# Optimization experiments

Measured on AMD Instinct MI355X. Metric: run time of the kernel, lower is better.

Reference implementation:

```python
import jax, jax.numpy as jnp
import numpy as np

B, T, C, H = 128, 512, 128, 64  # batch, seq, n_embd, head_size


def setup_inputs() -> dict:
    key = jax.random.key(0)
    ks = jax.random.split(key, 6)
    s = 1.0 / np.sqrt(C)
    return {
        "x": jax.random.normal(ks[0], (B, T, C), dtype=jnp.float32),
        "Wg": jax.random.normal(ks[1], (C, C), dtype=jnp.float32) * s,
        "bg": jnp.zeros((C,), dtype=jnp.float32),
        "Wk": jax.random.normal(ks[2], (C, H), dtype=jnp.float32) * s,
        "Wq": jax.random.normal(ks[3], (C, H), dtype=jnp.float32) * s,
        "Wv": jax.random.normal(ks[4], (C, H), dtype=jnp.float32) * s,
    }


def reference(x, Wg, bg, Wk, Wq, Wv):
    # GateLayer: x * sigmoid(Linear(x))
    g = jax.nn.sigmoid(jnp.einsum('btc,cd->btd', x, Wg) + bg)
    xg = x * g
    k = jnp.einsum('btc,ch->bth', xg, Wk)
    q = jnp.einsum('btc,ch->bth', xg, Wq)
    v = jnp.einsum('btc,ch->bth', xg, Wv)
    # NOTE: original scales by C**-0.5 (n_embd), not head_size**-0.5
    scale = C ** -0.5
    wei = jnp.einsum('bqh,bkh->bqk', q, k) * scale  # [B,T,T]
    causal = jnp.tril(jnp.ones((T, T), dtype=bool))
    wei = jnp.where(causal, wei, -jnp.inf)
    wei = jax.nn.softmax(wei, axis=-1)
    # dropout is identity in eval mode
    out = jnp.einsum('bqk,bkh->bqh', wei, v)  # [B,T,H]
    return out
```

## Files before the change

kernel.cpp:

```cpp
#include <hip/hip_runtime.h>


#define BB 128
#define TB 512
#define CC 128
#define HH 64

static constexpr float SCALE = 0.088388347648318447f;

typedef __attribute__((ext_vector_type(8))) short bf16x8;
typedef __attribute__((ext_vector_type(8))) unsigned short u16x8;
typedef __attribute__((ext_vector_type(4))) float f32x4;

__device__ inline unsigned short f2bf(float f) {
    union { float f; unsigned u; } x; x.f = f;
    unsigned r = x.u + 0x7fff + ((x.u >> 16) & 1);
    return (unsigned short)(r >> 16);
}
__device__ inline float bf2f(unsigned short h) {
    union { unsigned u; float f; } x; x.u = ((unsigned)h) << 16;
    return x.f;
}

__global__ void prep_weights(const float* __restrict__ Wg, const float* __restrict__ Wk,
                             const float* __restrict__ Wq, const float* __restrict__ Wv,
                             unsigned short* __restrict__ WgT, unsigned short* __restrict__ WkT,
                             unsigned short* __restrict__ WqT, unsigned short* __restrict__ WvT)
{
    int idx = blockIdx.x * 256 + threadIdx.x;
    if (idx < 16384) {
        int n = idx >> 7, k = idx & 127;
        WgT[idx] = f2bf(Wg[k * CC + n]);
    } else {
        int j = idx - 16384;
        int mtx = j >> 13;
        int r = j & 8191;
        int n = r >> 7, k = r & 127;
        const float* W = (mtx == 0) ? Wk : (mtx == 1) ? Wq : Wv;
        unsigned short* WT = (mtx == 0) ? WkT : (mtx == 1) ? WqT : WvT;
        WT[r] = f2bf(W[k * HH + n]);
    }
}

__global__ __launch_bounds__(256, 3) void gate_qkv_kernel(
    const float* __restrict__ x, const float* __restrict__ bg,
    const unsigned short* __restrict__ WgT, const unsigned short* __restrict__ WkT,
    const unsigned short* __restrict__ WqT, const unsigned short* __restrict__ WvT,
    unsigned short* __restrict__ qo, unsigned short* __restrict__ ko,
    unsigned short* __restrict__ vto)
{
    __shared__ unsigned short xsb[128 * 136];

    const int tid  = threadIdx.x;
    const int wv   = tid >> 6;
    const int lane = tid & 63;
    const int l15  = lane & 15;
    const int quad = lane >> 4;
    const int R0   = blockIdx.x * 128;

#pragma unroll
    for (int it = 0; it < 16; ++it) {
        int fid = tid + 256 * it;
        int r = fid >> 5, c4 = fid & 31;
        float4 xv = *(const float4*)(x + (size_t)(R0 + r) * CC + c4 * 4);
        ushort4 h;
        h.x = f2bf(xv.x); h.y = f2bf(xv.y); h.z = f2bf(xv.z); h.w = f2bf(xv.w);
        *(ushort4*)(xsb + r * 136 + c4 * 4) = h;
    }
    __syncthreads();

    bf16x8 bx[2][4];
#pragma unroll
    for (int mt = 0; mt < 2; ++mt)
#pragma unroll
        for (int kc = 0; kc < 4; ++kc)
            bx[mt][kc] = *(const bf16x8*)(xsb + (32 * wv + 16 * mt + l15) * 136 +
                                          kc * 32 + quad * 8);

    f32x4 acc[8][2];
#pragma unroll
    for (int nt = 0; nt < 8; ++nt)
#pragma unroll
        for (int mt = 0; mt < 2; ++mt) acc[nt][mt] = (f32x4){0.f, 0.f, 0.f, 0.f};

#pragma unroll
    for (int nt = 0; nt < 8; ++nt) {
        bf16x8 aw[4];
#pragma unroll
        for (int kc = 0; kc < 4; ++kc)
            aw[kc] = *(const bf16x8*)(WgT + (16 * nt + l15) * CC + kc * 32 + quad * 8);
#pragma unroll
        for (int mt = 0; mt < 2; ++mt)
#pragma unroll
            for (int kc = 0; kc < 4; ++kc)
                acc[nt][mt] = __builtin_amdgcn_mfma_f32_16x16x32_bf16(
                    aw[kc], bx[mt][kc], acc[nt][mt], 0, 0, 0);
    }

#pragma unroll
    for (int nt = 0; nt < 8; ++nt) {
        float4 bgv = *(const float4*)(bg + 16 * nt + quad * 4);
#pragma unroll
        for (int mt = 0; mt < 2; ++mt) {
            int m = 32 * wv + 16 * mt + l15;
            unsigned short* p = xsb + m * 136 + 16 * nt + quad * 4;
            ushort4 xb = *(const ushort4*)p;
            float s0 = acc[nt][mt][0] + bgv.x;
            float s1 = acc[nt][mt][1] + bgv.y;
            float s2 = acc[nt][mt][2] + bgv.z;
            float s3 = acc[nt][mt][3] + bgv.w;
            ushort4 o;
            o.x = f2bf(bf2f(xb.x) / (1.f + __expf(-s0)));
            o.y = f2bf(bf2f(xb.y) / (1.f + __expf(-s1)));
            o.z = f2bf(bf2f(xb.z) / (1.f + __expf(-s2)));
            o.w = f2bf(bf2f(xb.w) / (1.f + __expf(-s3)));
            *(ushort4*)p = o;
        }
    }
    __syncthreads();

#pragma unroll
    for (int mt = 0; mt < 2; ++mt)
#pragma unroll
        for (int kc = 0; kc < 4; ++kc)
            bx[mt][kc] = *(const bf16x8*)(xsb + (32 * wv + 16 * mt + l15) * 136 +
                                          kc * 32 + quad * 8);

    const int b = R0 >> 9, t0 = R0 & 511;
    for (int pj = 0; pj < 3; ++pj) {
        const unsigned short* WT = (pj == 0) ? WkT : (pj == 1) ? WqT : WvT;
        f32x4 pacc[4][2];
#pragma unroll
        for (int nt = 0; nt < 4; ++nt)
#pragma unroll
            for (int mt = 0; mt < 2; ++mt) pacc[nt][mt] = (f32x4){0.f, 0.f, 0.f, 0.f};

#pragma unroll
        for (int nt = 0; nt < 4; ++nt) {
            bf16x8 aw[4];
#pragma unroll
            for (int kc = 0; kc < 4; ++kc)
                aw[kc] = *(const bf16x8*)(WT + (16 * nt + l15) * CC + kc * 32 + quad * 8);
#pragma unroll
            for (int mt = 0; mt < 2; ++mt)
#pragma unroll
                for (int kc = 0; kc < 4; ++kc)
                    pacc[nt][mt] = __builtin_amdgcn_mfma_f32_16x16x32_bf16(
                        aw[kc], bx[mt][kc], pacc[nt][mt], 0, 0, 0);
        }

        if (pj < 2) {
            unsigned short* O = (pj == 0) ? ko : qo;
#pragma unroll
            for (int nt = 0; nt < 4; ++nt)
#pragma unroll
                for (int mt = 0; mt < 2; ++mt) {
                    int m = 32 * wv + 16 * mt + l15;
                    ushort4 h;
                    h.x = f2bf(pacc[nt][mt][0]);
                    h.y = f2bf(pacc[nt][mt][1]);
                    h.z = f2bf(pacc[nt][mt][2]);
                    h.w = f2bf(pacc[nt][mt][3]);
                    *(ushort4*)(O + (size_t)(R0 + m) * HH + 16 * nt + quad * 4) = h;
                }
        } else {
#pragma unroll
            for (int nt = 0; nt < 4; ++nt)
#pragma unroll
                for (int mt = 0; mt < 2; ++mt) {
                    int m = 32 * wv + 16 * mt + l15;
                    unsigned short* dst =
                        vto + (size_t)b * (HH * TB) + (16 * nt + quad * 4) * TB + t0 + m;
#pragma unroll
                    for (int r = 0; r < 4; ++r)
                        dst[r * TB] = f2bf(pacc[nt][mt][r]);
                }
        }
    }
}

__global__ __launch_bounds__(256) void attn_kernel(
    const unsigned short* __restrict__ q, const unsigned short* __restrict__ k,
    const unsigned short* __restrict__ vt, float* __restrict__ out)
{
    __shared__ unsigned short ks[64 * 72];
    __shared__ unsigned short vs[64 * 72];
    __shared__ unsigned short ps[64 * 76];

    const int tid  = threadIdx.x;
    const int wave = tid >> 6;
    const int lane = tid & 63;
    const int l15  = lane & 15;
    const int quad = lane >> 4;
    const int pr   = blockIdx.x;
    const int b    = blockIdx.y;
    const size_t base = (size_t)b * TB * HH;

    for (int pass = 0; pass < 2; ++pass) {
        const int qt = pass ? (7 - pr) : pr;
        const int q0 = qt * 64;

        const unsigned short* qrow = q + base + (size_t)(q0 + 16 * wave + l15) * HH;
        bf16x8 aq0 = *(const bf16x8*)(qrow + quad * 8);
        bf16x8 aq1 = *(const bf16x8*)(qrow + 32 + quad * 8);

        f32x4 o4[4];
        float mrow[4], lrow[4];
#pragma unroll
        for (int nt = 0; nt < 4; ++nt) o4[nt] = (f32x4){0.f, 0.f, 0.f, 0.f};
#pragma unroll
        for (int r = 0; r < 4; ++r) { mrow[r] = -1e30f; lrow[r] = 0.f; }

        for (int kt = 0; kt <= qt; ++kt) {
            const int k0 = kt * 64;
            __syncthreads();
#pragma unroll
            for (int i = 0; i < 2; ++i) {
                int cid = tid + 256 * i;
                int r = cid >> 3, c8 = cid & 7;
                *(bf16x8*)(ks + r * 72 + c8 * 8) =
                    *(const bf16x8*)(k + base + (size_t)(k0 + r) * HH + c8 * 8);
                *(bf16x8*)(vs + r * 72 + c8 * 8) =
                    *(const bf16x8*)(vt + base + (size_t)r * TB + k0 + c8 * 8);
            }
            __syncthreads();

            f32x4 s[4];
#pragma unroll
            for (int nt = 0; nt < 4; ++nt) {
                bf16x8 bk0 = *(const bf16x8*)(ks + (16 * nt + l15) * 72 + quad * 8);
                bf16x8 bk1 = *(const bf16x8*)(ks + (16 * nt + l15) * 72 + 32 + quad * 8);
                f32x4 z = (f32x4){0.f, 0.f, 0.f, 0.f};
                z = __builtin_amdgcn_mfma_f32_16x16x32_bf16(aq0, bk0, z, 0, 0, 0);
                z = __builtin_amdgcn_mfma_f32_16x16x32_bf16(aq1, bk1, z, 0, 0, 0);
                s[nt] = z;
            }

            const bool diag = (kt == qt);
            float mx[4];
#pragma unroll
            for (int r = 0; r < 4; ++r) mx[r] = -1e30f;
#pragma unroll
            for (int nt = 0; nt < 4; ++nt)
#pragma unroll
                for (int r = 0; r < 4; ++r) {
                    float sv = s[nt][r] * SCALE;
                    if (diag && (16 * nt + l15) > (16 * wave + quad * 4 + r)) sv = -1e30f;
                    s[nt][r] = sv;
                    mx[r] = fmaxf(mx[r], sv);
                }

#pragma unroll
            for (int r = 0; r < 4; ++r) {
                mx[r] = fmaxf(mx[r], __shfl_xor(mx[r], 1));
                mx[r] = fmaxf(mx[r], __shfl_xor(mx[r], 2));
                mx[r] = fmaxf(mx[r], __shfl_xor(mx[r], 4));
                mx[r] = fmaxf(mx[r], __shfl_xor(mx[r], 8));
            }
            float alpha[4], psum[4];
#pragma unroll
            for (int r = 0; r < 4; ++r) {
                float mn = fmaxf(mrow[r], mx[r]);
                alpha[r] = __expf(mrow[r] - mn);
                mrow[r] = mn;
                psum[r] = 0.f;
            }
#pragma unroll
            for (int nt = 0; nt < 4; ++nt)
#pragma unroll
                for (int r = 0; r < 4; ++r) {
                    float e = __expf(s[nt][r] - mrow[r]);
                    psum[r] += e;
                    ps[(16 * wave + quad * 4 + r) * 76 + 16 * nt + l15] = f2bf(e);
                }
#pragma unroll
            for (int r = 0; r < 4; ++r) {
                psum[r] += __shfl_xor(psum[r], 1);
                psum[r] += __shfl_xor(psum[r], 2);
                psum[r] += __shfl_xor(psum[r], 4);
                psum[r] += __shfl_xor(psum[r], 8);
                lrow[r] = lrow[r] * alpha[r] + psum[r];
            }
#pragma unroll
            for (int nt = 0; nt < 4; ++nt)
#pragma unroll
                for (int r = 0; r < 4; ++r) o4[nt][r] *= alpha[r];

            bf16x8 ap0 = *(const bf16x8*)(ps + (16 * wave + l15) * 76 + quad * 8);
            bf16x8 ap1 = *(const bf16x8*)(ps + (16 * wave + l15) * 76 + 32 + quad * 8);
#pragma unroll
            for (int nt = 0; nt < 4; ++nt) {
                bf16x8 bv0 = *(const bf16x8*)(vs + (16 * nt + l15) * 72 + quad * 8);
                bf16x8 bv1 = *(const bf16x8*)(vs + (16 * nt + l15) * 72 + 32 + quad * 8);
                o4[nt] = __builtin_amdgcn_mfma_f32_16x16x32_bf16(ap0, bv0, o4[nt], 0, 0, 0);
                o4[nt] = __builtin_amdgcn_mfma_f32_16x16x32_bf16(ap1, bv1, o4[nt], 0, 0, 0);
            }
        }

        float inv[4];
#pragma unroll
        for (int r = 0; r < 4; ++r) inv[r] = 1.f / lrow[r];
#pragma unroll
        for (int nt = 0; nt < 4; ++nt)
#pragma unroll
            for (int r = 0; r < 4; ++r)
                out[base + (size_t)(q0 + 16 * wave + quad * 4 + r) * HH + 16 * nt + l15] =
                    o4[nt][r] * inv[r];
    }
}

extern "C" void kernel_launch(void* const* d_in, const int* in_sizes, int n_in,
                              void* d_out, int out_size, void* d_ws, size_t ws_size,
                              hipStream_t stream) {
    const float* x  = (const float*)d_in[0];
    const float* Wg = (const float*)d_in[1];
    const float* bg = (const float*)d_in[2];
    const float* Wk = (const float*)d_in[3];
    const float* Wq = (const float*)d_in[4];
    const float* Wv = (const float*)d_in[5];
    float* out = (float*)d_out;

    unsigned short* ws = (unsigned short*)d_ws;
    const size_t BTH = (size_t)BB * TB * HH;
    unsigned short* qo  = ws;
    unsigned short* ko  = ws + BTH;
    unsigned short* vto = ws + 2 * BTH;
    unsigned short* WgT = ws + 3 * BTH;
    unsigned short* WkT = WgT + 16384;
    unsigned short* WqT = WkT + 8192;
    unsigned short* WvT = WqT + 8192;

    hipLaunchKernelGGL(prep_weights, dim3(160), dim3(256), 0, stream,
                       Wg, Wk, Wq, Wv, WgT, WkT, WqT, WvT);
    hipLaunchKernelGGL(gate_qkv_kernel, dim3(BB * TB / 128), dim3(256), 0, stream,
                       x, bg, WgT, WkT, WqT, WvT, qo, ko, vto);
    hipLaunchKernelGGL(attn_kernel, dim3(4, BB), dim3(256), 0, stream,
                       qo, ko, vto, out);
}
```

Measured before the change: 137.5 us.

## Halve gate tile, stage V transpose through LDS, one query tile per attention block

The gate/QKV kernel now handles 64 rows per block instead of 128, with one 16-row MFMA tile per wave. This drops the second __syncthreads and lets occupancy rise to 4 blocks. V is written transposed through shared memory so the global stores become 16-byte vectors instead of scattered 2-byte stores, and the sigmoid divide is replaced by a hardware reciprocal. The attention kernel drops the paired-tile load-balancing scheme and launches 8 query tiles per batch, one per block. This doubles the grid size but makes block work uneven, ordered heaviest first.

```diff
diff --git a/kernel.cpp b/kernel.cpp
--- a/kernel.cpp
+++ b/kernel.cpp
@@ -42,24 +42,24 @@
     }
 }
 
-__global__ __launch_bounds__(256, 3) void gate_qkv_kernel(
+__global__ __launch_bounds__(256, 4) void gate_qkv_kernel(
     const float* __restrict__ x, const float* __restrict__ bg,
     const unsigned short* __restrict__ WgT, const unsigned short* __restrict__ WkT,
     const unsigned short* __restrict__ WqT, const unsigned short* __restrict__ WvT,
     unsigned short* __restrict__ qo, unsigned short* __restrict__ ko,
     unsigned short* __restrict__ vto)
 {
-    __shared__ unsigned short xsb[128 * 136];
+    __shared__ unsigned short xsb[64 * 136];
 
     const int tid  = threadIdx.x;
     const int wv   = tid >> 6;
     const int lane = tid & 63;
     const int l15  = lane & 15;
     const int quad = lane >> 4;
-    const int R0   = blockIdx.x * 128;
-
-#pragma unroll
-    for (int it = 0; it < 16; ++it) {
+    const int R0   = blockIdx.x * 64;
+
+#pragma unroll
+    for (int it = 0; it < 8; ++it) {
         int fid = tid + 256 * it;
         int r = fid >> 5, c4 = fid & 31;
         float4 xv = *(const float4*)(x + (size_t)(R0 + r) * CC + c4 * 4);
@@ -69,117 +69,93 @@
     }
     __syncthreads();
 
-    bf16x8 bx[2][4];
-#pragma unroll
-    for (int mt = 0; mt < 2; ++mt)
-#pragma unroll
-        for (int kc = 0; kc < 4; ++kc)
-            bx[mt][kc] = *(const bf16x8*)(xsb + (32 * wv + 16 * mt + l15) * 136 +
-                                          kc * 32 + quad * 8);
-
-    f32x4 acc[8][2];
-#pragma unroll
-    for (int nt = 0; nt < 8; ++nt)
-#pragma unroll
-        for (int mt = 0; mt < 2; ++mt) acc[nt][mt] = (f32x4){0.f, 0.f, 0.f, 0.f};
-
+    const int m = 16 * wv + l15;
+
+    bf16x8 bx[4];
+#pragma unroll
+    for (int kc = 0; kc < 4; ++kc)
+        bx[kc] = *(const bf16x8*)(xsb + m * 136 + kc * 32 + quad * 8);
+
+    f32x4 acc[8];
+#pragma unroll
+    for (int nt = 0; nt < 8; ++nt) acc[nt] = (f32x4){0.f, 0.f, 0.f, 0.f};
 #pragma unroll
     for (int nt = 0; nt < 8; ++nt) {
-        bf16x8 aw[4];
-#pragma unroll
-        for (int kc = 0; kc < 4; ++kc)
-            aw[kc] = *(const bf16x8*)(WgT + (16 * nt + l15) * CC + kc * 32 + quad * 8);
-#pragma unroll
-        for (int mt = 0; mt < 2; ++mt)
-#pragma unroll
-            for (int kc = 0; kc < 4; ++kc)
-                acc[nt][mt] = __builtin_amdgcn_mfma_f32_16x16x32_bf16(
-                    aw[kc], bx[mt][kc], acc[nt][mt], 0, 0, 0);
+#pragma unroll
+        for (int kc = 0; kc < 4; ++kc) {
+            bf16x8 aw = *(const bf16x8*)(WgT + (16 * nt + l15) * CC + kc * 32 + quad * 8);
+            acc[nt] = __builtin_amdgcn_mfma_f32_16x16x32_bf16(aw, bx[kc], acc[nt], 0, 0, 0);
+        }
     }
 
 #pragma unroll
     for (int nt = 0; nt < 8; ++nt) {
         float4 bgv = *(const float4*)(bg + 16 * nt + quad * 4);
-#pragma unroll
-        for (int mt = 0; mt < 2; ++mt) {
-            int m = 32 * wv + 16 * mt + l15;
-            unsigned short* p = xsb + m * 136 + 16 * nt + quad * 4;
-            ushort4 xb = *(const ushort4*)p;
-            float s0 = acc[nt][mt][0] + bgv.x;
-            float s1 = acc[nt][mt][1] + bgv.y;
-            float s2 = acc[nt][mt][2] + bgv.z;
-            float s3 = acc[nt][mt][3] + bgv.w;
-            ushort4 o;
-            o.x = f2bf(bf2f(xb.x) / (1.f + __expf(-s0)));
-            o.y = f2bf(bf2f(xb.y) / (1.f + __expf(-s1)));
-            o.z = f2bf(bf2f(xb.z) / (1.f + __expf(-s2)));
-            o.w = f2bf(bf2f(xb.w) / (1.f + __expf(-s3)));
-            *(ushort4*)p = o;
-        }
-    }
-    __syncthreads();
-
-#pragma unroll
-    for (int mt = 0; mt < 2; ++mt)
-#pragma unroll
-        for (int kc = 0; kc < 4; ++kc)
-            bx[mt][kc] = *(const bf16x8*)(xsb + (32 * wv + 16 * mt + l15) * 136 +
-                                          kc * 32 + quad * 8);
+        unsigned short* p = xsb + m * 136 + 16 * nt + quad * 4;
+        ushort4 xb = *(const ushort4*)p;
+        float e0 = __expf(-(acc[nt][0] + bgv.x));
+        float e1 = __expf(-(acc[nt][1] + bgv.y));
+        float e2 = __expf(-(acc[nt][2] + bgv.z));
+        float e3 = __expf(-(acc[nt][3] + bgv.w));
+        ushort4 o;
+        o.x = f2bf(bf2f(xb.x) * __builtin_amdgcn_rcpf(1.f + e0));
+        o.y = f2bf(bf2f(xb.y) * __builtin_amdgcn_rcpf(1.f + e1));
+        o.z = f2bf(bf2f(xb.z) * __builtin_amdgcn_rcpf(1.f + e2));
+        o.w = f2bf(bf2f(xb.w) * __builtin_amdgcn_rcpf(1.f + e3));
+        *(ushort4*)p = o;
+    }
+
+#pragma unroll
+    for (int kc = 0; kc < 4; ++kc)
+        bx[kc] = *(const bf16x8*)(xsb + m * 136 + kc * 32 + quad * 8);
 
     const int b = R0 >> 9, t0 = R0 & 511;
     for (int pj = 0; pj < 3; ++pj) {
         const unsigned short* WT = (pj == 0) ? WkT : (pj == 1) ? WqT : WvT;
-        f32x4 pacc[4][2];
-#pragma unroll
-        for (int nt = 0; nt < 4; ++nt)
-#pragma unroll
-            for (int mt = 0; mt < 2; ++mt) pacc[nt][mt] = (f32x4){0.f, 0.f, 0.f, 0.f};
-
+        f32x4 pacc[4];
+#pragma unroll
+        for (int nt = 0; nt < 4; ++nt) pacc[nt] = (f32x4){0.f, 0.f, 0.f, 0.f};
 #pragma unroll
         for (int nt = 0; nt < 4; ++nt) {
-            bf16x8 aw[4];
-#pragma unroll
-            for (int kc = 0; kc < 4; ++kc)
-                aw[kc] = *(const bf16x8*)(WT + (16 * nt + l15) * CC + kc * 32 + quad * 8);
-#pragma unroll
-            for (int mt = 0; mt < 2; ++mt)
-#pragma unroll
-                for (int kc = 0; kc < 4; ++kc)
-                    pacc[nt][mt] = __builtin_amdgcn_mfma_f32_16x16x32_bf16(
-                        aw[kc], bx[mt][kc], pacc[nt][mt], 0, 0, 0);
+#pragma unroll
+            for (int kc = 0; kc < 4; ++kc) {
+                bf16x8 aw = *(const bf16x8*)(WT + (16 * nt + l15) * CC + kc * 32 + quad * 8);
+                pacc[nt] = __builtin_amdgcn_mfma_f32_16x16x32_bf16(aw, bx[kc], pacc[nt], 0, 0, 0);
+            }
         }
 
         if (pj < 2) {
             unsigned short* O = (pj == 0) ? ko : qo;
 #pragma unroll
-            for (int nt = 0; nt < 4; ++nt)
-#pragma unroll
-                for (int mt = 0; mt < 2; ++mt) {
-                    int m = 32 * wv + 16 * mt + l15;
-                    ushort4 h;
-                    h.x = f2bf(pacc[nt][mt][0]);
-                    h.y = f2bf(pacc[nt][mt][1]);
-                    h.z = f2bf(pacc[nt][mt][2]);
-                    h.w = f2bf(pacc[nt][mt][3]);
-                    *(ushort4*)(O + (size_t)(R0 + m) * HH + 16 * nt + quad * 4) = h;
-                }
+            for (int nt = 0; nt < 4; ++nt) {
+                ushort4 h;
+                h.x = f2bf(pacc[nt][0]); h.y = f2bf(pacc[nt][1]);
+                h.z = f2bf(pacc[nt][2]); h.w = f2bf(pacc[nt][3]);
+                *(ushort4*)(O + (size_t)(R0 + m) * HH + 16 * nt + quad * 4) = h;
+            }
         } else {
 #pragma unroll
-            for (int nt = 0; nt < 4; ++nt)
-#pragma unroll
-                for (int mt = 0; mt < 2; ++mt) {
-                    int m = 32 * wv + 16 * mt + l15;
-                    unsigned short* dst =
-                        vto + (size_t)b * (HH * TB) + (16 * nt + quad * 4) * TB + t0 + m;
-#pragma unroll
-                    for (int r = 0; r < 4; ++r)
-                        dst[r * TB] = f2bf(pacc[nt][mt][r]);
-                }
-        }
-    }
-}
-
-__global__ __launch_bounds__(256) void attn_kernel(
+            for (int nt = 0; nt < 4; ++nt) {
+                ushort4 h;
+                h.x = f2bf(pacc[nt][0]); h.y = f2bf(pacc[nt][1]);
+                h.z = f2bf(pacc[nt][2]); h.w = f2bf(pacc[nt][3]);
+                *(ushort4*)(xsb + m * 136 + 16 * nt + quad * 4) = h;
+            }
+            const int h = tid & 63, tc = tid >> 6;
+            u16x8 v0, v1;
+#pragma unroll
+            for (int j = 0; j < 8; ++j) {
+                v0[j] = xsb[(16 * tc + j) * 136 + h];
+                v1[j] = xsb[(16 * tc + 8 + j) * 136 + h];
+            }
+            unsigned short* dst = vto + (size_t)b * (HH * TB) + h * TB + t0 + 16 * tc;
+            *(u16x8*)(dst)     = v0;
+            *(u16x8*)(dst + 8) = v1;
+        }
+    }
+}
+
+__global__ __launch_bounds__(256, 4) void attn_kernel(
     const unsigned short* __restrict__ q, const unsigned short* __restrict__ k,
     const unsigned short* __restrict__ vt, float* __restrict__ out)
 {
@@ -192,121 +168,117 @@
     const int lane = tid & 63;
     const int l15  = lane & 15;
     const int quad = lane >> 4;
-    const int pr   = blockIdx.x;
+    const int qt   = 7 - blockIdx.x;
     const int b    = blockIdx.y;
+    const int q0   = qt * 64;
     const size_t base = (size_t)b * TB * HH;
 
-    for (int pass = 0; pass < 2; ++pass) {
-        const int qt = pass ? (7 - pr) : pr;
-        const int q0 = qt * 64;
-
-        const unsigned short* qrow = q + base + (size_t)(q0 + 16 * wave + l15) * HH;
-        bf16x8 aq0 = *(const bf16x8*)(qrow + quad * 8);
-        bf16x8 aq1 = *(const bf16x8*)(qrow + 32 + quad * 8);
-
-        f32x4 o4[4];
-        float mrow[4], lrow[4];
-#pragma unroll
-        for (int nt = 0; nt < 4; ++nt) o4[nt] = (f32x4){0.f, 0.f, 0.f, 0.f};
-#pragma unroll
-        for (int r = 0; r < 4; ++r) { mrow[r] = -1e30f; lrow[r] = 0.f; }
-
-        for (int kt = 0; kt <= qt; ++kt) {
-            const int k0 = kt * 64;
-            __syncthreads();
-#pragma unroll
-            for (int i = 0; i < 2; ++i) {
-                int cid = tid + 256 * i;
-                int r = cid >> 3, c8 = cid & 7;
-                *(bf16x8*)(ks + r * 72 + c8 * 8) =
-                    *(const bf16x8*)(k + base + (size_t)(k0 + r) * HH + c8 * 8);
-                *(bf16x8*)(vs + r * 72 + c8 * 8) =
-                    *(const bf16x8*)(vt + base + (size_t)r * TB + k0 + c8 * 8);
-            }
-            __syncthreads();
-
-            f32x4 s[4];
-#pragma unroll
-            for (int nt = 0; nt < 4; ++nt) {
-                bf16x8 bk0 = *(const bf16x8*)(ks + (16 * nt + l15) * 72 + quad * 8);
-                bf16x8 bk1 = *(const bf16x8*)(ks + (16 * nt + l15) * 72 + 32 + quad * 8);
-                f32x4 z = (f32x4){0.f, 0.f, 0.f, 0.f};
-                z = __builtin_amdgcn_mfma_f32_16x16x32_bf16(aq0, bk0, z, 0, 0, 0);
-                z = __builtin_amdgcn_mfma_f32_16x16x32_bf16(aq1, bk1, z, 0, 0, 0);
-                s[nt] = z;
-            }
-
-            const bool diag = (kt == qt);
-            float mx[4];
-#pragma unroll
-            for (int r = 0; r < 4; ++r) mx[r] = -1e30f;
-#pragma unroll
-            for (int nt = 0; nt < 4; ++nt)
-#pragma unroll
-                for (int r = 0; r < 4; ++r) {
-                    float sv = s[nt][r] * SCALE;
-                    if (diag && (16 * nt + l15) > (16 * wave + quad * 4 + r)) sv = -1e30f;
-                    s[nt][r] = sv;
-                    mx[r] = fmaxf(mx[r], sv);
-                }
-
+    const unsigned short* qrow = q + base + (size_t)(q0 + 16 * wave + l15) * HH;
+    bf16x8 aq0 = *(const bf16x8*)(qrow + quad * 8);
+    bf16x8 aq1 = *(const bf16x8*)(qrow + 32 + quad * 8);
+
+    f32x4 o4[4];
+    float mrow[4], lrow[4];
+#pragma unroll
+    for (int nt = 0; nt < 4; ++nt) o4[nt] = (f32x4){0.f, 0.f, 0.f, 0.f};
+#pragma unroll
+    for (int r = 0; r < 4; ++r) { mrow[r] = -1e30f; lrow[r] = 0.f; }
+
+    for (int kt = 0; kt <= qt; ++kt) {
+        const int k0 = kt * 64;
+        __syncthreads();
+#pragma unroll
+        for (int i = 0; i < 2; ++i) {
+            int cid = tid + 256 * i;
+            int r = cid >> 3, c8 = cid & 7;
+            *(bf16x8*)(ks + r * 72 + c8 * 8) =
+                *(const bf16x8*)(k + base + (size_t)(k0 + r) * HH + c8 * 8);
+            *(bf16x8*)(vs + r * 72 + c8 * 8) =
+                *(const bf16x8*)(vt + base + (size_t)r * TB + k0 + c8 * 8);
+        }
+        __syncthreads();
+
+        f32x4 s[4];
+#pragma unroll
+        for (int nt = 0; nt < 4; ++nt) {
+            bf16x8 bk0 = *(const bf16x8*)(ks + (16 * nt + l15) * 72 + quad * 8);
+            bf16x8 bk1 = *(const bf16x8*)(ks + (16 * nt + l15) * 72 + 32 + quad * 8);
+            f32x4 z = (f32x4){0.f, 0.f, 0.f, 0.f};
+            z = __builtin_amdgcn_mfma_f32_16x16x32_bf16(aq0, bk0, z, 0, 0, 0);
+            z = __builtin_amdgcn_mfma_f32_16x16x32_bf16(aq1, bk1, z, 0, 0, 0);
+            s[nt] = z;
+        }
+
+        const bool diag = (kt == qt);
+        float mx[4];
+#pragma unroll
+        for (int r = 0; r < 4; ++r) mx[r] = -1e30f;
+#pragma unroll
+        for (int nt = 0; nt < 4; ++nt)
 #pragma unroll
             for (int r = 0; r < 4; ++r) {
-                mx[r] = fmaxf(mx[r], __shfl_xor(mx[r], 1));
-                mx[r] = fmaxf(mx[r], __shfl_xor(mx[r], 2));
-                mx[r] = fmaxf(mx[r], __shfl_xor(mx[r], 4));
-                mx[r] = fmaxf(mx[r], __shfl_xor(mx[r], 8));
-            }
-            float alpha[4], psum[4];
+                float sv = s[nt][r] * SCALE;
+                if (diag && (16 * nt + l15) > (16 * wave + quad * 4 + r)) sv = -1e30f;
+                s[nt][r] = sv;
+                mx[r] = fmaxf(mx[r], sv);
+            }
+
+#pragma unroll
+        for (int r = 0; r < 4; ++r) {
+            mx[r] = fmaxf(mx[r], __shfl_xor(mx[r], 1));
+            mx[r] = fmaxf(mx[r], __shfl_xor(mx[r], 2));
+            mx[r] = fmaxf(mx[r], __shfl_xor(mx[r], 4));
+            mx[r] = fmaxf(mx[r], __shfl_xor(mx[r], 8));
+        }
+        float alpha[4], psum[4];
+#pragma unroll
+        for (int r = 0; r < 4; ++r) {
+            float mn = fmaxf(mrow[r], mx[r]);
+            alpha[r] = __expf(mrow[r] - mn);
+            mrow[r] = mn;
+            psum[r] = 0.f;
+        }
+#pragma unroll
+        for (int nt = 0; nt < 4; ++nt)
 #pragma unroll
             for (int r = 0; r < 4; ++r) {
-                float mn = fmaxf(mrow[r], mx[r]);
-                alpha[r] = __expf(mrow[r] - mn);
-                mrow[r] = mn;
-                psum[r] = 0.f;
-            }
-#pragma unroll
-            for (int nt = 0; nt < 4; ++nt)
-#pragma unroll
-                for (int r = 0; r < 4; ++r) {
-                    float e = __expf(s[nt][r] - mrow[r]);
-                    psum[r] += e;
-                    ps[(16 * wave + quad * 4 + r) * 76 + 16 * nt + l15] = f2bf(e);
-                }
-#pragma unroll
-            for (int r = 0; r < 4; ++r) {
-                psum[r] += __shfl_xor(psum[r], 1);
-                psum[r] += __shfl_xor(psum[r], 2);
-                psum[r] += __shfl_xor(psum[r], 4);
-                psum[r] += __shfl_xor(psum[r], 8);
-                lrow[r] = lrow[r] * alpha[r] + psum[r];
-            }
-#pragma unroll
-            for (int nt = 0; nt < 4; ++nt)
-#pragma unroll
-                for (int r = 0; r < 4; ++r) o4[nt][r] *= alpha[r];
-
-            bf16x8 ap0 = *(const bf16x8*)(ps + (16 * wave + l15) * 76 + quad * 8);
-            bf16x8 ap1 = *(const bf16x8*)(ps + (16 * wave + l15) * 76 + 32 + quad * 8);
-#pragma unroll
-            for (int nt = 0; nt < 4; ++nt) {
-                bf16x8 bv0 = *(const bf16x8*)(vs + (16 * nt + l15) * 72 + quad * 8);
-                bf16x8 bv1 = *(const bf16x8*)(vs + (16 * nt + l15) * 72 + 32 + quad * 8);
-                o4[nt] = __builtin_amdgcn_mfma_f32_16x16x32_bf16(ap0, bv0, o4[nt], 0, 0, 0);
-                o4[nt] = __builtin_amdgcn_mfma_f32_16x16x32_bf16(ap1, bv1, o4[nt], 0, 0, 0);
-            }
-        }
-
-        float inv[4];
-#pragma unroll
-        for (int r = 0; r < 4; ++r) inv[r] = 1.f / lrow[r];
+                float e = __expf(s[nt][r] - mrow[r]);
+                psum[r] += e;
+                ps[(16 * wave + quad * 4 + r) * 76 + 16 * nt + l15] = f2bf(e);
+            }
+#pragma unroll
+        for (int r = 0; r < 4; ++r) {
+            psum[r] += __shfl_xor(psum[r], 1);
+            psum[r] += __shfl_xor(psum[r], 2);
+            psum[r] += __shfl_xor(psum[r], 4);
+            psum[r] += __shfl_xor(psum[r], 8);
+            lrow[r] = lrow[r] * alpha[r] + psum[r];
+        }
 #pragma unroll
         for (int nt = 0; nt < 4; ++nt)
 #pragma unroll
-            for (int r = 0; r < 4; ++r)
-                out[base + (size_t)(q0 + 16 * wave + quad * 4 + r) * HH + 16 * nt + l15] =
-                    o4[nt][r] * inv[r];
-    }
+            for (int r = 0; r < 4; ++r) o4[nt][r] *= alpha[r];
+
+        bf16x8 ap0 = *(const bf16x8*)(ps + (16 * wave + l15) * 76 + quad * 8);
+        bf16x8 ap1 = *(const bf16x8*)(ps + (16 * wave + l15) * 76 + 32 + quad * 8);
+#pragma unroll
+        for (int nt = 0; nt < 4; ++nt) {
+            bf16x8 bv0 = *(const bf16x8*)(vs + (16 * nt + l15) * 72 + quad * 8);
+            bf16x8 bv1 = *(const bf16x8*)(vs + (16 * nt + l15) * 72 + 32 + quad * 8);
+            o4[nt] = __builtin_amdgcn_mfma_f32_16x16x32_bf16(ap0, bv0, o4[nt], 0, 0, 0);
+            o4[nt] = __builtin_amdgcn_mfma_f32_16x16x32_bf16(ap1, bv1, o4[nt], 0, 0, 0);
+        }
+    }
+
+    float inv[4];
+#pragma unroll
+    for (int r = 0; r < 4; ++r) inv[r] = __builtin_amdgcn_rcpf(lrow[r]);
+#pragma unroll
+    for (int nt = 0; nt < 4; ++nt)
+#pragma unroll
+        for (int r = 0; r < 4; ++r)
+            out[base + (size_t)(q0 + 16 * wave + quad * 4 + r) * HH + 16 * nt + l15] =
+                o4[nt][r] * inv[r];
 }
 
 extern "C" void kernel_launch(void* const* d_in, const int* in_sizes, int n_in,
@@ -332,8 +304,8 @@
 
     hipLaunchKernelGGL(prep_weights, dim3(160), dim3(256), 0, stream,
                        Wg, Wk, Wq, Wv, WgT, WkT, WqT, WvT);
-    hipLaunchKernelGGL(gate_qkv_kernel, dim3(BB * TB / 128), dim3(256), 0, stream,
+    hipLaunchKernelGGL(gate_qkv_kernel, dim3(BB * TB / 64), dim3(256), 0, stream,
                        x, bg, WgT, WkT, WqT, WvT, qo, ko, vto);
-    hipLaunchKernelGGL(attn_kernel, dim3(4, BB), dim3(256), 0, stream,
+    hipLaunchKernelGGL(attn_kernel, dim3(8, BB), dim3(256), 0, stream,
                        qo, ko, vto, out);
 }
```

Result: slower. 160.9 us (+17.0%).

## Prefetch K/V tiles into registers and merge two query passes into one loop

Applied to the files above, without the earlier changes.

The attention kernel's two passes over query tiles pr and 7-pr become a single flat loop of nine K/V tile iterations. The next tile's K and V are loaded into registers while the current tile is being computed, so global-load latency overlaps the MFMA and softmax work. The gate's divisions and the final normalisation are swapped for the hardware reciprocal instruction. The cost is extra register pressure and slightly lower precision from the approximate rcp.

```diff
diff --git a/kernel.cpp b/kernel.cpp
--- a/kernel.cpp
+++ b/kernel.cpp
@@ -105,15 +105,15 @@
             int m = 32 * wv + 16 * mt + l15;
             unsigned short* p = xsb + m * 136 + 16 * nt + quad * 4;
             ushort4 xb = *(const ushort4*)p;
-            float s0 = acc[nt][mt][0] + bgv.x;
-            float s1 = acc[nt][mt][1] + bgv.y;
-            float s2 = acc[nt][mt][2] + bgv.z;
-            float s3 = acc[nt][mt][3] + bgv.w;
+            float e0 = __expf(-(acc[nt][mt][0] + bgv.x));
+            float e1 = __expf(-(acc[nt][mt][1] + bgv.y));
+            float e2 = __expf(-(acc[nt][mt][2] + bgv.z));
+            float e3 = __expf(-(acc[nt][mt][3] + bgv.w));
             ushort4 o;
-            o.x = f2bf(bf2f(xb.x) / (1.f + __expf(-s0)));
-            o.y = f2bf(bf2f(xb.y) / (1.f + __expf(-s1)));
-            o.z = f2bf(bf2f(xb.z) / (1.f + __expf(-s2)));
-            o.w = f2bf(bf2f(xb.w) / (1.f + __expf(-s3)));
+            o.x = f2bf(bf2f(xb.x) * __builtin_amdgcn_rcpf(1.f + e0));
+            o.y = f2bf(bf2f(xb.y) * __builtin_amdgcn_rcpf(1.f + e1));
+            o.z = f2bf(bf2f(xb.z) * __builtin_amdgcn_rcpf(1.f + e2));
+            o.w = f2bf(bf2f(xb.w) * __builtin_amdgcn_rcpf(1.f + e3));
             *(ushort4*)p = o;
         }
     }
@@ -157,10 +157,8 @@
                 for (int mt = 0; mt < 2; ++mt) {
                     int m = 32 * wv + 16 * mt + l15;
                     ushort4 h;
-                    h.x = f2bf(pacc[nt][mt][0]);
-                    h.y = f2bf(pacc[nt][mt][1]);
-                    h.z = f2bf(pacc[nt][mt][2]);
-                    h.w = f2bf(pacc[nt][mt][3]);
+                    h.x = f2bf(pacc[nt][mt][0]); h.y = f2bf(pacc[nt][mt][1]);
+                    h.z = f2bf(pacc[nt][mt][2]); h.w = f2bf(pacc[nt][mt][3]);
                     *(ushort4*)(O + (size_t)(R0 + m) * HH + 16 * nt + quad * 4) = h;
                 }
         } else {
@@ -195,117 +193,140 @@
     const int pr   = blockIdx.x;
     const int b    = blockIdx.y;
     const size_t base = (size_t)b * TB * HH;
-
-    for (int pass = 0; pass < 2; ++pass) {
-        const int qt = pass ? (7 - pr) : pr;
-        const int q0 = qt * 64;
-
-        const unsigned short* qrow = q + base + (size_t)(q0 + 16 * wave + l15) * HH;
-        bf16x8 aq0 = *(const bf16x8*)(qrow + quad * 8);
-        bf16x8 aq1 = *(const bf16x8*)(qrow + 32 + quad * 8);
-
-        f32x4 o4[4];
-        float mrow[4], lrow[4];
-#pragma unroll
-        for (int nt = 0; nt < 4; ++nt) o4[nt] = (f32x4){0.f, 0.f, 0.f, 0.f};
-#pragma unroll
-        for (int r = 0; r < 4; ++r) { mrow[r] = -1e30f; lrow[r] = 0.f; }
-
-        for (int kt = 0; kt <= qt; ++kt) {
-            const int k0 = kt * 64;
-            __syncthreads();
-#pragma unroll
-            for (int i = 0; i < 2; ++i) {
-                int cid = tid + 256 * i;
-                int r = cid >> 3, c8 = cid & 7;
-                *(bf16x8*)(ks + r * 72 + c8 * 8) =
-                    *(const bf16x8*)(k + base + (size_t)(k0 + r) * HH + c8 * 8);
-                *(bf16x8*)(vs + r * 72 + c8 * 8) =
-                    *(const bf16x8*)(vt + base + (size_t)r * TB + k0 + c8 * 8);
+    const int qtA = pr;
+
+    const int r0 = tid >> 3,          c80 = (tid & 7) * 8;
+    const int r1 = (tid + 256) >> 3,  c81 = (tid & 7) * 8;
+
+    bf16x8 kr0 = *(const bf16x8*)(k + base + (size_t)r0 * HH + c80);
+    bf16x8 kr1 = *(const bf16x8*)(k + base + (size_t)r1 * HH + c81);
+    bf16x8 vr0 = *(const bf16x8*)(vt + base + (size_t)r0 * TB + c80);
+    bf16x8 vr1 = *(const bf16x8*)(vt + base + (size_t)r1 * TB + c81);
+
+    int qt = qtA, q0 = qtA * 64;
+    const unsigned short* qrow = q + base + (size_t)(q0 + 16 * wave + l15) * HH;
+    bf16x8 aq0 = *(const bf16x8*)(qrow + quad * 8);
+    bf16x8 aq1 = *(const bf16x8*)(qrow + 32 + quad * 8);
+
+    f32x4 o4[4];
+    float mrow[4], lrow[4];
+#pragma unroll
+    for (int nt = 0; nt < 4; ++nt) o4[nt] = (f32x4){0.f, 0.f, 0.f, 0.f};
+#pragma unroll
+    for (int r = 0; r < 4; ++r) { mrow[r] = -1e30f; lrow[r] = 0.f; }
+
+    for (int it = 0; it < 9; ++it) {
+        const int kt = (it <= qtA) ? it : it - qtA - 1;
+
+        __syncthreads();
+        *(bf16x8*)(ks + r0 * 72 + c80) = kr0;
+        *(bf16x8*)(ks + r1 * 72 + c81) = kr1;
+        *(bf16x8*)(vs + r0 * 72 + c80) = vr0;
+        *(bf16x8*)(vs + r1 * 72 + c81) = vr1;
+        __syncthreads();
+
+        if (it < 8) {
+            const int itn = it + 1;
+            const int ktn = (itn <= qtA) ? itn : itn - qtA - 1;
+            const int k0n = ktn * 64;
+            kr0 = *(const bf16x8*)(k + base + (size_t)(k0n + r0) * HH + c80);
+            kr1 = *(const bf16x8*)(k + base + (size_t)(k0n + r1) * HH + c81);
+            vr0 = *(const bf16x8*)(vt + base + (size_t)r0 * TB + k0n + c80);
+            vr1 = *(const bf16x8*)(vt + base + (size_t)r1 * TB + k0n + c81);
+        }
+
+        f32x4 s[4];
+#pragma unroll
+        for (int nt = 0; nt < 4; ++nt) {
+            bf16x8 bk0 = *(const bf16x8*)(ks + (16 * nt + l15) * 72 + quad * 8);
+            bf16x8 bk1 = *(const bf16x8*)(ks + (16 * nt + l15) * 72 + 32 + quad * 8);
+            f32x4 z = (f32x4){0.f, 0.f, 0.f, 0.f};
+            z = __builtin_amdgcn_mfma_f32_16x16x32_bf16(aq0, bk0, z, 0, 0, 0);
+            z = __builtin_amdgcn_mfma_f32_16x16x32_bf16(aq1, bk1, z, 0, 0, 0);
+            s[nt] = z;
+        }
+
+        const bool diag = (kt == qt);
+        float mx[4];
+#pragma unroll
+        for (int r = 0; r < 4; ++r) mx[r] = -1e30f;
+#pragma unroll
+        for (int nt = 0; nt < 4; ++nt)
+#pragma unroll
+            for (int r = 0; r < 4; ++r) {
+                float sv = s[nt][r] * SCALE;
+                if (diag && (16 * nt + l15) > (16 * wave + quad * 4 + r)) sv = -1e30f;
+                s[nt][r] = sv;
+                mx[r] = fmaxf(mx[r], sv);
             }
-            __syncthreads();
-
-            f32x4 s[4];
-#pragma unroll
-            for (int nt = 0; nt < 4; ++nt) {
-                bf16x8 bk0 = *(const bf16x8*)(ks + (16 * nt + l15) * 72 + quad * 8);
-                bf16x8 bk1 = *(const bf16x8*)(ks + (16 * nt + l15) * 72 + 32 + quad * 8);
-                f32x4 z = (f32x4){0.f, 0.f, 0.f, 0.f};
-                z = __builtin_amdgcn_mfma_f32_16x16x32_bf16(aq0, bk0, z, 0, 0, 0);
-                z = __builtin_amdgcn_mfma_f32_16x16x32_bf16(aq1, bk1, z, 0, 0, 0);
-                s[nt] = z;
+
+#pragma unroll
+        for (int r = 0; r < 4; ++r) {
+            mx[r] = fmaxf(mx[r], __shfl_xor(mx[r], 1));
+            mx[r] = fmaxf(mx[r], __shfl_xor(mx[r], 2));
+            mx[r] = fmaxf(mx[r], __shfl_xor(mx[r], 4));
+            mx[r] = fmaxf(mx[r], __shfl_xor(mx[r], 8));
+        }
+        float alpha[4], psum[4];
+#pragma unroll
+        for (int r = 0; r < 4; ++r) {
+            float mn = fmaxf(mrow[r], mx[r]);
+            alpha[r] = __expf(mrow[r] - mn);
+            mrow[r] = mn;
+            psum[r] = 0.f;
+        }
+#pragma unroll
+        for (int nt = 0; nt < 4; ++nt)
+#pragma unroll
+            for (int r = 0; r < 4; ++r) {
+                float e = __expf(s[nt][r] - mrow[r]);
+                psum[r] += e;
+                ps[(16 * wave + quad * 4 + r) * 76 + 16 * nt + l15] = f2bf(e);
             }
-
-            const bool diag = (kt == qt);
-            float mx[4];
-#pragma unroll
-            for (int r = 0; r < 4; ++r) mx[r] = -1e30f;
+#pragma unroll
+        for (int r = 0; r < 4; ++r) {
+            psum[r] += __shfl_xor(psum[r], 1);
+            psum[r] += __shfl_xor(psum[r], 2);
+            psum[r] += __shfl_xor(psum[r], 4);
+            psum[r] += __shfl_xor(psum[r], 8);
+            lrow[r] = lrow[r] * alpha[r] + psum[r];
+        }
+#pragma unroll
+        for (int nt = 0; nt < 4; ++nt)
+#pragma unroll
+            for (int r = 0; r < 4; ++r) o4[nt][r] *= alpha[r];
+
+        bf16x8 ap0 = *(const bf16x8*)(ps + (16 * wave + l15) * 76 + quad * 8);
+        bf16x8 ap1 = *(const bf16x8*)(ps + (16 * wave + l15) * 76 + 32 + quad * 8);
+#pragma unroll
+        for (int nt = 0; nt < 4; ++nt) {
+            bf16x8 bv0 = *(const bf16x8*)(vs + (16 * nt + l15) * 72 + quad * 8);
+            bf16x8 bv1 = *(const bf16x8*)(vs + (16 * nt + l15) * 72 + 32 + quad * 8);
+            o4[nt] = __builtin_amdgcn_mfma_f32_16x16x32_bf16(ap0, bv0, o4[nt], 0, 0, 0);
+            o4[nt] = __builtin_amdgcn_mfma_f32_16x16x32_bf16(ap1, bv1, o4[nt], 0, 0, 0);
+        }
+
+        if (kt == qt) {
+            float inv[4];
+#pragma unroll
+            for (int r = 0; r < 4; ++r) inv[r] = __builtin_amdgcn_rcpf(lrow[r]);
 #pragma unroll
             for (int nt = 0; nt < 4; ++nt)
 #pragma unroll
-                for (int r = 0; r < 4; ++r) {
-                    float sv = s[nt][r] * SCALE;
-                    if (diag && (16 * nt + l15) > (16 * wave + quad * 4 + r)) sv = -1e30f;
-                    s[nt][r] = sv;
-                    mx[r] = fmaxf(mx[r], sv);
-                }
-
-#pragma unroll
-            for (int r = 0; r < 4; ++r) {
-                mx[r] = fmaxf(mx[r], __shfl_xor(mx[r], 1));
-                mx[r] = fmaxf(mx[r], __shfl_xor(mx[r], 2));
-                mx[r] = fmaxf(mx[r], __shfl_xor(mx[r], 4));
-                mx[r] = fmaxf(mx[r], __shfl_xor(mx[r], 8));
+                for (int r = 0; r < 4; ++r)
+                    out[base + (size_t)(q0 + 16 * wave + quad * 4 + r) * HH + 16 * nt + l15] =
+                        o4[nt][r] * inv[r];
+            if (it < 8) {
+                qt = 7 - pr; q0 = qt * 64;
+                const unsigned short* qrow2 = q + base + (size_t)(q0 + 16 * wave + l15) * HH;
+                aq0 = *(const bf16x8*)(qrow2 + quad * 8);
+                aq1 = *(const bf16x8*)(qrow2 + 32 + quad * 8);
+#pragma unroll
+                for (int nt = 0; nt < 4; ++nt) o4[nt] = (f32x4){0.f, 0.f, 0.f, 0.f};
+#pragma unroll
+                for (int r = 0; r < 4; ++r) { mrow[r] = -1e30f; lrow[r] = 0.f; }
             }
-            float alpha[4], psum[4];
-#pragma unroll
-            for (int r = 0; r < 4; ++r) {
-                float mn = fmaxf(mrow[r], mx[r]);
-                alpha[r] = __expf(mrow[r] - mn);
-                mrow[r] = mn;
-                psum[r] = 0.f;
-            }
-#pragma unroll
-            for (int nt = 0; nt < 4; ++nt)
-#pragma unroll
-                for (int r = 0; r < 4; ++r) {
-                    float e = __expf(s[nt][r] - mrow[r]);
-                    psum[r] += e;
-                    ps[(16 * wave + quad * 4 + r) * 76 + 16 * nt + l15] = f2bf(e);
-                }
-#pragma unroll
-            for (int r = 0; r < 4; ++r) {
-                psum[r] += __shfl_xor(psum[r], 1);
-                psum[r] += __shfl_xor(psum[r], 2);
-                psum[r] += __shfl_xor(psum[r], 4);
-                psum[r] += __shfl_xor(psum[r], 8);
-                lrow[r] = lrow[r] * alpha[r] + psum[r];
-            }
-#pragma unroll
-            for (int nt = 0; nt < 4; ++nt)
-#pragma unroll
-                for (int r = 0; r < 4; ++r) o4[nt][r] *= alpha[r];
-
-            bf16x8 ap0 = *(const bf16x8*)(ps + (16 * wave + l15) * 76 + quad * 8);
-            bf16x8 ap1 = *(const bf16x8*)(ps + (16 * wave + l15) * 76 + 32 + quad * 8);
-#pragma unroll
-            for (int nt = 0; nt < 4; ++nt) {
-                bf16x8 bv0 = *(const bf16x8*)(vs + (16 * nt + l15) * 72 + quad * 8);
-                bf16x8 bv1 = *(const bf16x8*)(vs + (16 * nt + l15) * 72 + 32 + quad * 8);
-                o4[nt] = __builtin_amdgcn_mfma_f32_16x16x32_bf16(ap0, bv0, o4[nt], 0, 0, 0);
-                o4[nt] = __builtin_amdgcn_mfma_f32_16x16x32_bf16(ap1, bv1, o4[nt], 0, 0, 0);
-            }
-        }
-
-        float inv[4];
-#pragma unroll
-        for (int r = 0; r < 4; ++r) inv[r] = 1.f / lrow[r];
-#pragma unroll
-        for (int nt = 0; nt < 4; ++nt)
-#pragma unroll
-            for (int r = 0; r < 4; ++r)
-                out[base + (size_t)(q0 + 16 * wave + quad * 4 + r) * HH + 16 * nt + l15] =
-                    o4[nt][r] * inv[r];
+        }
     }
 }
 
```

Measured after the change: 133.4 us. 1.03x faster.
